# Optimization experiments

Measured on AMD Instinct MI355X. Metric: run time of the kernel, lower is better.

## Reference

```python
import jax, jax.numpy as jnp
import numpy as np

N = 10000      # nodes
E = 320000     # edges (avg degree 32)
D = 512        # input features
H = 2048       # dim_hidden hard-coded in module
C = 40         # num_classes


def setup_inputs() -> dict:
    key = jax.random.key(0)
    k = jax.random.split(key, 4)
    x = jax.random.normal(k[0], (N, D), dtype=jnp.float32)
    edge_index = jax.random.randint(k[1], (2, E), 0, N)
    W1 = jax.random.normal(k[2], (D, H), dtype=jnp.float32) * (1.0 / np.sqrt(D))
    b1 = jnp.zeros((H,), jnp.float32)
    W2 = jax.random.normal(k[3], (H, C), dtype=jnp.float32) * (1.0 / np.sqrt(H))
    b2 = jnp.zeros((C,), jnp.float32)
    return {"x": x, "edge_index": edge_index, "W1": W1, "b1": b1, "W2": W2, "b2": b2}


def _sym_norm(edge_index, n):
    # GCN symmetric normalization with self-loops: deg includes the self loop.
    src, dst = edge_index[0], edge_index[1]
    deg = jnp.zeros((n,), jnp.float32).at[dst].add(1.0) + 1.0
    dinv = jax.lax.rsqrt(deg)
    return src, dst, dinv


def _propagate(h, src, dst, dinv):
    # out[i] = sum_{j->i} dinv[j]*dinv[i]*h[j]  +  dinv[i]^2 * h[i] (self loop)
    coef = (dinv[src] * dinv[dst])[:, None]            # [E,1]
    agg = jax.ops.segment_sum(h[src] * coef, dst, num_segments=h.shape[0])
    return agg + h * (dinv * dinv)[:, None]


def _gcn_conv(x, W, b, src, dst, dinv):
    # A_hat (X W) == (A_hat X) W; aggregate in the smaller feature dim.
    if W.shape[0] <= W.shape[1]:
        return _propagate(x, src, dst, dinv) @ W + b
    return _propagate(x @ W, src, dst, dinv) + b


def reference(x, edge_index, W1, b1, W2, b2):
    src, dst, dinv = _sym_norm(edge_index, x.shape[0])
    h = jax.nn.relu(_gcn_conv(x, W1, b1, src, dst, dinv))
    return _gcn_conv(h, W2, b2, src, dst, dinv)
```

## Files before the change

kernel.cpp:

```cpp
#include <hip/hip_runtime.h>
#include <stdint.h>

#define N_NODES 10000
#define N_EDGES 320000
#define D_IN    512
#define D_HID   2048
#define N_CLS   40
#define MP1     10112
#define HSTR    136

typedef float f32x4  __attribute__((ext_vector_type(4)));
typedef short bf16x8 __attribute__((ext_vector_type(8)));
typedef unsigned short us8 __attribute__((ext_vector_type(8)));

__device__ inline unsigned short f2bf(float f){
  unsigned int u = __float_as_uint(f);
  u += 0x7fffu + ((u >> 16) & 1u);
  return (unsigned short)(u >> 16);
}

__device__ inline float bf2f(unsigned short h){
  return __uint_as_float(((unsigned int)h) << 16);
}

__device__ inline void gl_lds16(const void* g, void* l){
  __builtin_amdgcn_global_load_lds((const __attribute__((address_space(1))) void*)g,
                                   (__attribute__((address_space(3))) void*)l, 16, 0, 0);
}

__global__ void k_prep0(const float* __restrict__ x, unsigned short* __restrict__ Xb,
                        const int* __restrict__ ei, int* __restrict__ deg){
  if (blockIdx.x < 2500){
    int idx = blockIdx.x*256 + threadIdx.x;
    const f32x4* x4 = (const f32x4*)x;
    f32x4 a = x4[idx*2], b = x4[idx*2+1];
    us8 o;
    o[0]=f2bf(a.x); o[1]=f2bf(a.y); o[2]=f2bf(a.z); o[3]=f2bf(a.w);
    o[4]=f2bf(b.x); o[5]=f2bf(b.y); o[6]=f2bf(b.z); o[7]=f2bf(b.w);
    *(us8*)(Xb + (size_t)idx*8) = o;
  } else {
    int e = (blockIdx.x - 2500)*256 + threadIdx.x;
    if (e < N_EDGES) atomicAdd(&deg[ei[N_EDGES + e]], 1);
  }
}

__global__ void k_scan(const int* __restrict__ deg, int* __restrict__ offsets,
                       int* __restrict__ cursor, float* __restrict__ dinv){
  __shared__ int sums[1024];
  const int t = threadIdx.x;
  const int CH = 10;
  int base = t*CH;
  int local[CH]; int s = 0;
  for (int j = 0; j < CH; j++){
    int v = (base + j < N_NODES) ? deg[base + j] : 0;
    local[j] = s; s += v;
    if (base + j < N_NODES) dinv[base + j] = rsqrtf((float)v + 1.0f);
  }
  sums[t] = s;
  __syncthreads();
  for (int off = 1; off < 1024; off <<= 1){
    int v = (t >= off) ? sums[t - off] : 0;
    __syncthreads();
    sums[t] += v;
    __syncthreads();
  }
  int pre = (t > 0) ? sums[t-1] : 0;
  for (int j = 0; j < CH; j++){
    int idx = base + j;
    if (idx < N_NODES){ int o = pre + local[j]; offsets[idx] = o; cursor[idx] = o; }
  }
}

__global__ void k_fill(const int* __restrict__ ei, int* __restrict__ cursor, int* __restrict__ csr_src){
  int e = blockIdx.x*256 + threadIdx.x;
  if (e < N_EDGES){
    int s = ei[e], d = ei[N_EDGES + e];
    int pos = atomicAdd(&cursor[d], 1);
    csr_src[pos] = s;
  }
}

__global__ __launch_bounds__(256) void k_gjoint(const unsigned short* __restrict__ Xb,
                          const int* __restrict__ csr_src,
                          const int* __restrict__ offsets, const int* __restrict__ deg,
                          const float* __restrict__ dinv, unsigned short* __restrict__ Pb,
                          const float* __restrict__ W1, unsigned short* __restrict__ Wt1,
                          const float* __restrict__ W2, unsigned short* __restrict__ Wt2){
  __shared__ float tile[32][33];
  if (blockIdx.x < 2500){
    const int w    = threadIdx.x >> 6;
    const int lane = threadIdx.x & 63;
    const int i    = blockIdx.x*4 + w;
    const float di = dinv[i];
    float acc[8];
    us8 xi = *(const us8*)(Xb + (size_t)i*D_IN + lane*8);
    const float dii = di*di;
    #pragma unroll
    for (int r = 0; r < 8; r++) acc[r] = dii * bf2f(xi[r]);
    const int start = offsets[i], cnt = deg[i];
    for (int c0 = 0; c0 < cnt; c0 += 64){
      int m = cnt - c0; if (m > 64) m = 64;
      int s = 0; float cf = 0.0f;
      if (lane < m){ s = csr_src[start + c0 + lane]; cf = dinv[s]*di; }
      for (int j = 0; j < m; j++){
        int   sj = __shfl(s, j);
        float cj = __shfl(cf, j);
        us8 xr = *(const us8*)(Xb + (size_t)sj*D_IN + lane*8);
        #pragma unroll
        for (int r = 0; r < 8; r++) acc[r] += cj * bf2f(xr[r]);
      }
    }
    us8 o;
    #pragma unroll
    for (int r = 0; r < 8; r++) o[r] = f2bf(acc[r]);
    *(us8*)(Pb + (size_t)i*D_IN + lane*8) = o;
  } else if (blockIdx.x < 2500 + 1024){
    const int bb = blockIdx.x - 2500;
    const int n0 = (bb & 63)*32, k0 = (bb >> 6)*32;
    const int tx = threadIdx.x & 31, ty = threadIdx.x >> 5;
    for (int i = 0; i < 32; i += 8)
      tile[ty+i][tx] = W1[(size_t)(k0+ty+i)*D_HID + n0+tx];
    __syncthreads();
    for (int i = 0; i < 32; i += 8)
      Wt1[(size_t)(n0+ty+i)*D_IN + k0+tx] = f2bf(tile[tx][ty+i]);
  } else {
    int idx = (blockIdx.x - 3524)*256 + threadIdx.x;
    if (idx < 48*D_HID){
      int n = idx >> 11, k = idx & (D_HID-1);
      Wt2[idx] = (n < N_CLS) ? f2bf(W2[k*N_CLS + n]) : (unsigned short)0;
    }
  }
}

__global__ __launch_bounds__(256) void k_gemm1f(const unsigned short* __restrict__ Pb,
                                                const unsigned short* __restrict__ Wt1,
                                                const float* __restrict__ b1,
                                                const unsigned short* __restrict__ Wt2,
                                                float* __restrict__ G){
  __shared__ short smem[128*HSTR];
  short* As = smem;
  short* Bs = smem + 4096;
  short* Hs = smem;
  const int t    = threadIdx.x;
  const int lane = t & 63;
  const int wid  = t >> 6;
  const int wm   = (wid >> 1)*64, wn = (wid & 1)*64;
  const int m0   = blockIdx.x*128, n0 = blockIdx.y*128;
  const int arow = t >> 2;
  const int akof = ((t & 3) ^ ((t >> 3) & 3))*8;
  const int fr   = lane & 15;
  const int q    = lane >> 4;
  const int sq8  = (q ^ ((fr >> 1) & 3))*8;
  f32x4 acc[4][4] = {};
  for (int kb = 0; kb < D_IN; kb += 32){
    gl_lds16(Pb  + (size_t)(m0 +      arow)*D_IN + kb + akof, As + t*8);
    gl_lds16(Pb  + (size_t)(m0 + 64 + arow)*D_IN + kb + akof, As + 2048 + t*8);
    gl_lds16(Wt1 + (size_t)(n0 +      arow)*D_IN + kb + akof, Bs + t*8);
    gl_lds16(Wt1 + (size_t)(n0 + 64 + arow)*D_IN + kb + akof, Bs + 2048 + t*8);
    __syncthreads();
    bf16x8 a[4], b[4];
    #pragma unroll
    for (int i = 0; i < 4; i++) a[i] = *(const bf16x8*)(As + (wm + i*16 + fr)*32 + sq8);
    #pragma unroll
    for (int j = 0; j < 4; j++) b[j] = *(const bf16x8*)(Bs + (wn + j*16 + fr)*32 + sq8);
    #pragma unroll
    for (int i = 0; i < 4; i++)
      #pragma unroll
      for (int j = 0; j < 4; j++)
        acc[i][j] = __builtin_amdgcn_mfma_f32_16x16x32_bf16(a[i], b[j], acc[i][j], 0, 0, 0);
    __syncthreads();
  }
  #pragma unroll
  for (int j = 0; j < 4; j++){
    int col = wn + j*16 + fr;
    float bias = b1[n0 + col];
    #pragma unroll
    for (int i = 0; i < 4; i++){
      int rbase = wm + i*16 + q*4;
      f32x4 v = acc[i][j];
      #pragma unroll
      for (int r = 0; r < 4; r++){
        float h = fmaxf(v[r] + bias, 0.0f);
        Hs[(rbase + r)*HSTR + col] = (short)f2bf(h);
      }
    }
  }
  __syncthreads();
  f32x4 acc2[2][3] = {};
  for (int ks = 0; ks < 4; ks++){
    bf16x8 a2[2];
    #pragma unroll
    for (int i2 = 0; i2 < 2; i2++)
      a2[i2] = *(const bf16x8*)(Hs + (wid*32 + i2*16 + fr)*HSTR + ks*32 + q*8);
    #pragma unroll
    for (int j2 = 0; j2 < 3; j2++){
      bf16x8 b2 = *(const bf16x8*)(Wt2 + (size_t)(j2*16 + fr)*D_HID + n0 + ks*32 + q*8);
      #pragma unroll
      for (int i2 = 0; i2 < 2; i2++)
        acc2[i2][j2] = __builtin_amdgcn_mfma_f32_16x16x32_bf16(a2[i2], b2, acc2[i2][j2], 0, 0, 0);
    }
  }
  #pragma unroll
  for (int j2 = 0; j2 < 3; j2++){
    int col = j2*16 + fr;
    if (col < N_CLS){
      #pragma unroll
      for (int i2 = 0; i2 < 2; i2++){
        int rbase = m0 + wid*32 + i2*16 + q*4;
        f32x4 v = acc2[i2][j2];
        #pragma unroll
        for (int r = 0; r < 4; r++){
          int row = rbase + r;
          if (row < N_NODES)
            atomicAdd(&G[row*N_CLS + col], v[r]);
        }
      }
    }
  }
}

__global__ void k_gather2(const float* __restrict__ G, const int* __restrict__ csr_src,
                          const int* __restrict__ offsets, const int* __restrict__ deg,
                          const float* __restrict__ dinv, const float* __restrict__ b2,
                          float* __restrict__ out){
  __shared__ int   ssrc[64];
  __shared__ float scoef[64];
  const int i = blockIdx.x;
  const int t = threadIdx.x;
  const float di = dinv[i];
  const int start = offsets[i], cnt = deg[i];
  float acc = 0.0f;
  if (t < N_CLS) acc = di*di * G[i*N_CLS + t];
  for (int c0 = 0; c0 < cnt; c0 += 64){
    int m = cnt - c0; if (m > 64) m = 64;
    if (t < m){
      int s = csr_src[start + c0 + t];
      ssrc[t] = s; scoef[t] = dinv[s]*di;
    }
    __syncthreads();
    if (t < N_CLS)
      for (int j = 0; j < m; j++)
        acc += scoef[j] * G[ssrc[j]*N_CLS + t];
    __syncthreads();
  }
  if (t < N_CLS) out[i*N_CLS + t] = acc + b2[t];
}

extern "C" void kernel_launch(void* const* d_in, const int* in_sizes, int n_in,
                              void* d_out, int out_size, void* d_ws, size_t ws_size,
                              hipStream_t stream){
  const float* x  = (const float*)d_in[0];
  const int*   ei = (const int*)d_in[1];
  const float* W1 = (const float*)d_in[2];
  const float* b1 = (const float*)d_in[3];
  const float* W2 = (const float*)d_in[4];
  const float* b2 = (const float*)d_in[5];
  float* out = (float*)d_out;

  char* ws = (char*)d_ws;
  size_t off = 0;
  auto alloc = [&](size_t bytes) -> void* {
    void* p = ws + off; off += (bytes + 255) & ~(size_t)255; return p;
  };
  int*   deg     = (int*)alloc((size_t)N_NODES*4);
  float* dinv    = (float*)alloc((size_t)N_NODES*4);
  int*   offsets = (int*)alloc((size_t)N_NODES*4);
  int*   cursor  = (int*)alloc((size_t)N_NODES*4);
  int*   csr     = (int*)alloc((size_t)N_EDGES*4);
  unsigned short* Xb  = (unsigned short*)alloc((size_t)N_NODES*D_IN*2);
  unsigned short* Pb  = (unsigned short*)alloc((size_t)MP1*D_IN*2);
  unsigned short* Wt1 = (unsigned short*)alloc((size_t)D_HID*D_IN*2);
  unsigned short* Wt2 = (unsigned short*)alloc((size_t)48*D_HID*2);
  float* G = (float*)alloc((size_t)N_NODES*N_CLS*4);

  hipMemsetAsync(deg, 0, (size_t)N_NODES*4, stream);
  hipMemsetAsync(G,   0, (size_t)N_NODES*N_CLS*4, stream);

  k_prep0<<<2500 + 1250, 256, 0, stream>>>(x, Xb, ei, deg);
  k_scan<<<1, 1024, 0, stream>>>(deg, offsets, cursor, dinv);
  k_fill<<<(N_EDGES+255)/256, 256, 0, stream>>>(ei, cursor, csr);
  k_gjoint<<<2500 + 1024 + 384, 256, 0, stream>>>(Xb, csr, offsets, deg, dinv, Pb,
                                                  W1, Wt1, W2, Wt2);
  k_gemm1f<<<dim3(MP1/128, D_IN*4/128), 256, 0, stream>>>(Pb, Wt1, b1, Wt2, G);
  k_gather2<<<N_NODES, 64, 0, stream>>>(G, csr, offsets, deg, dinv, b2, out);
}
```

Measured before the change: 253.5 us.

## Double-buffer GEMM1 LDS tiles with direct-to-LDS prefetch and partial vmcnt waits

The GEMM1 main loop now ping-pongs between two LDS buffers, issuing the global-to-LDS loads for the next k-slice before computing the current one. It waits with a partial vmcnt so only the older loads must land, and replaces __syncthreads with raw s_barrier plus compiler memory fences. The aim is to hide global load latency behind the MFMA work. It relies on hand-encoded waitcnt immediates and on the 128*HSTR shared buffer being large enough for two 8192-short stages, which adds correctness risk.

```diff
diff --git a/kernel.cpp b/kernel.cpp
--- a/kernel.cpp
+++ b/kernel.cpp
@@ -138,8 +138,6 @@
                                                 const unsigned short* __restrict__ Wt2,
                                                 float* __restrict__ G){
   __shared__ short smem[128*HSTR];
-  short* As = smem;
-  short* Bs = smem + 4096;
   short* Hs = smem;
   const int t    = threadIdx.x;
   const int lane = t & 63;
@@ -151,13 +149,36 @@
   const int fr   = lane & 15;
   const int q    = lane >> 4;
   const int sq8  = (q ^ ((fr >> 1) & 3))*8;
+
+  const unsigned short* ApA = Pb  + (size_t)(m0 +      arow)*D_IN + akof;
+  const unsigned short* ApB = Pb  + (size_t)(m0 + 64 + arow)*D_IN + akof;
+  const unsigned short* BpA = Wt1 + (size_t)(n0 +      arow)*D_IN + akof;
+  const unsigned short* BpB = Wt1 + (size_t)(n0 + 64 + arow)*D_IN + akof;
+
   f32x4 acc[4][4] = {};
-  for (int kb = 0; kb < D_IN; kb += 32){
-    gl_lds16(Pb  + (size_t)(m0 +      arow)*D_IN + kb + akof, As + t*8);
-    gl_lds16(Pb  + (size_t)(m0 + 64 + arow)*D_IN + kb + akof, As + 2048 + t*8);
-    gl_lds16(Wt1 + (size_t)(n0 +      arow)*D_IN + kb + akof, Bs + t*8);
-    gl_lds16(Wt1 + (size_t)(n0 + 64 + arow)*D_IN + kb + akof, Bs + 2048 + t*8);
-    __syncthreads();
+  {
+    short* As = smem;       short* Bs = smem + 4096;
+    gl_lds16(ApA, As + t*8);  gl_lds16(ApB, As + 2048 + t*8);
+    gl_lds16(BpA, Bs + t*8);  gl_lds16(BpB, Bs + 2048 + t*8);
+  }
+  #pragma unroll
+  for (int ks = 0; ks < 16; ks++){
+    if (ks < 15){
+      short* As = smem + ((ks+1)&1)*8192;
+      short* Bs = As + 4096;
+      const int kb = (ks+1)*32;
+      gl_lds16(ApA + kb, As + t*8);  gl_lds16(ApB + kb, As + 2048 + t*8);
+      gl_lds16(BpA + kb, Bs + t*8);  gl_lds16(BpB + kb, Bs + 2048 + t*8);
+      asm volatile("" ::: "memory");
+      __builtin_amdgcn_s_waitcnt(0x0F74);
+    } else {
+      asm volatile("" ::: "memory");
+      __builtin_amdgcn_s_waitcnt(0x0F70);
+    }
+    __builtin_amdgcn_s_barrier();
+    asm volatile("" ::: "memory");
+    const short* As = smem + (ks&1)*8192;
+    const short* Bs = As + 4096;
     bf16x8 a[4], b[4];
     #pragma unroll
     for (int i = 0; i < 4; i++) a[i] = *(const bf16x8*)(As + (wm + i*16 + fr)*32 + sq8);
@@ -168,7 +189,9 @@
       #pragma unroll
       for (int j = 0; j < 4; j++)
         acc[i][j] = __builtin_amdgcn_mfma_f32_16x16x32_bf16(a[i], b[j], acc[i][j], 0, 0, 0);
-    __syncthreads();
+    asm volatile("" ::: "memory");
+    __builtin_amdgcn_s_barrier();
+    asm volatile("" ::: "memory");
   }
   #pragma unroll
   for (int j = 0; j < 4; j++){
```

Measured after the change: 242.0 us. 4.5% less time.

## Pre-swizzle GEMM operands into MFMA fragment layout and load directly to registers

Applied to the files above, without the earlier changes.

The aggregation and weight-transpose kernels now write A and B operands in a layout that matches the MFMA register fragments. The first GEMM then reads them straight from global memory into registers with a one-step register prefetch, dropping the LDS staging and both per-iteration barriers. The grid is transposed so that blocks sharing a weight column tile run adjacently, and launch bounds now request 3 blocks per CU. The cost is that each operand element is loaded separately by every wave that needs it, so reuse moves from LDS to L2/L1 and global traffic rises.

```diff
diff --git a/kernel.cpp b/kernel.cpp
--- a/kernel.cpp
+++ b/kernel.cpp
@@ -21,11 +21,6 @@
 
 __device__ inline float bf2f(unsigned short h){
   return __uint_as_float(((unsigned int)h) << 16);
-}
-
-__device__ inline void gl_lds16(const void* g, void* l){
-  __builtin_amdgcn_global_load_lds((const __attribute__((address_space(1))) void*)g,
-                                   (__attribute__((address_space(3))) void*)l, 16, 0, 0);
 }
 
 __global__ void k_prep0(const float* __restrict__ x, unsigned short* __restrict__ Xb,
@@ -83,8 +78,8 @@
 __global__ __launch_bounds__(256) void k_gjoint(const unsigned short* __restrict__ Xb,
                           const int* __restrict__ csr_src,
                           const int* __restrict__ offsets, const int* __restrict__ deg,
-                          const float* __restrict__ dinv, unsigned short* __restrict__ Pb,
-                          const float* __restrict__ W1, unsigned short* __restrict__ Wt1,
+                          const float* __restrict__ dinv, unsigned short* __restrict__ Afrag,
+                          const float* __restrict__ W1, unsigned short* __restrict__ Bfrag,
                           const float* __restrict__ W2, unsigned short* __restrict__ Wt2){
   __shared__ float tile[32][33];
   if (blockIdx.x < 2500){
@@ -113,7 +108,9 @@
     us8 o;
     #pragma unroll
     for (int r = 0; r < 8; r++) o[r] = f2bf(acc[r]);
-    *(us8*)(Pb + (size_t)i*D_IN + lane*8) = o;
+    const int mt = i >> 4, fr = i & 15;
+    const int ks = lane >> 2, q = lane & 3;
+    *(us8*)(Afrag + ((size_t)(mt*16 + ks)*64 + q*16 + fr)*8) = o;
   } else if (blockIdx.x < 2500 + 1024){
     const int bb = blockIdx.x - 2500;
     const int n0 = (bb & 63)*32, k0 = (bb >> 6)*32;
@@ -121,8 +118,14 @@
     for (int i = 0; i < 32; i += 8)
       tile[ty+i][tx] = W1[(size_t)(k0+ty+i)*D_HID + n0+tx];
     __syncthreads();
-    for (int i = 0; i < 32; i += 8)
-      Wt1[(size_t)(n0+ty+i)*D_IN + k0+tx] = f2bf(tile[tx][ty+i]);
+    const int ks = k0 >> 5;
+    for (int i = 0; i < 32; i += 8){
+      int n = n0 + ty + i;
+      int k = k0 + tx;
+      int p = n >> 7, jt = (n >> 4) & 7, fr = n & 15;
+      int q = (tx >> 3) & 3, e = tx & 7;
+      Bfrag[((((size_t)p*16 + ks)*8 + jt)*64 + q*16 + fr)*8 + e] = f2bf(tile[tx][ty+i]);
+    }
   } else {
     int idx = (blockIdx.x - 3524)*256 + threadIdx.x;
     if (idx < 48*D_HID){
@@ -132,44 +135,53 @@
   }
 }
 
-__global__ __launch_bounds__(256) void k_gemm1f(const unsigned short* __restrict__ Pb,
-                                                const unsigned short* __restrict__ Wt1,
-                                                const float* __restrict__ b1,
-                                                const unsigned short* __restrict__ Wt2,
-                                                float* __restrict__ G){
-  __shared__ short smem[128*HSTR];
-  short* As = smem;
-  short* Bs = smem + 4096;
-  short* Hs = smem;
+__global__ __launch_bounds__(256, 3) void k_gemm1f(const unsigned short* __restrict__ Afrag,
+                                                   const unsigned short* __restrict__ Bfrag,
+                                                   const float* __restrict__ b1,
+                                                   const unsigned short* __restrict__ Wt2,
+                                                   float* __restrict__ G){
+  __shared__ short Hs[128*HSTR];
   const int t    = threadIdx.x;
   const int lane = t & 63;
   const int wid  = t >> 6;
   const int wm   = (wid >> 1)*64, wn = (wid & 1)*64;
-  const int m0   = blockIdx.x*128, n0 = blockIdx.y*128;
-  const int arow = t >> 2;
-  const int akof = ((t & 3) ^ ((t >> 3) & 3))*8;
+  const int m0   = blockIdx.y*128, n0 = blockIdx.x*128;
   const int fr   = lane & 15;
   const int q    = lane >> 4;
-  const int sq8  = (q ^ ((fr >> 1) & 3))*8;
+
+  const int mtb = (m0 + wm) >> 4;
+  const int p   = blockIdx.x;
+  const int jtb = wn >> 4;
+  const unsigned short* Aw = Afrag + (size_t)lane*8;
+  const unsigned short* Bw = Bfrag + (size_t)lane*8;
+
   f32x4 acc[4][4] = {};
-  for (int kb = 0; kb < D_IN; kb += 32){
-    gl_lds16(Pb  + (size_t)(m0 +      arow)*D_IN + kb + akof, As + t*8);
-    gl_lds16(Pb  + (size_t)(m0 + 64 + arow)*D_IN + kb + akof, As + 2048 + t*8);
-    gl_lds16(Wt1 + (size_t)(n0 +      arow)*D_IN + kb + akof, Bs + t*8);
-    gl_lds16(Wt1 + (size_t)(n0 + 64 + arow)*D_IN + kb + akof, Bs + 2048 + t*8);
-    __syncthreads();
-    bf16x8 a[4], b[4];
-    #pragma unroll
-    for (int i = 0; i < 4; i++) a[i] = *(const bf16x8*)(As + (wm + i*16 + fr)*32 + sq8);
-    #pragma unroll
-    for (int j = 0; j < 4; j++) b[j] = *(const bf16x8*)(Bs + (wn + j*16 + fr)*32 + sq8);
+  bf16x8 ac[4], bc[4], an[4], bn[4];
+  #pragma unroll
+  for (int i = 0; i < 4; i++) ac[i] = *(const bf16x8*)(Aw + (size_t)(mtb + i)*8192);
+  #pragma unroll
+  for (int j = 0; j < 4; j++) bc[j] = *(const bf16x8*)(Bw + (size_t)((p*16 + 0)*8 + jtb + j)*512);
+
+  for (int ks = 0; ks < 16; ks++){
+    if (ks < 15){
+      #pragma unroll
+      for (int i = 0; i < 4; i++)
+        an[i] = *(const bf16x8*)(Aw + (size_t)((mtb + i)*16 + ks + 1)*512);
+      #pragma unroll
+      for (int j = 0; j < 4; j++)
+        bn[j] = *(const bf16x8*)(Bw + (size_t)((p*16 + ks + 1)*8 + jtb + j)*512);
+    }
     #pragma unroll
     for (int i = 0; i < 4; i++)
       #pragma unroll
       for (int j = 0; j < 4; j++)
-        acc[i][j] = __builtin_amdgcn_mfma_f32_16x16x32_bf16(a[i], b[j], acc[i][j], 0, 0, 0);
-    __syncthreads();
-  }
+        acc[i][j] = __builtin_amdgcn_mfma_f32_16x16x32_bf16(ac[i], bc[j], acc[i][j], 0, 0, 0);
+    #pragma unroll
+    for (int i = 0; i < 4; i++) ac[i] = an[i];
+    #pragma unroll
+    for (int j = 0; j < 4; j++) bc[j] = bn[j];
+  }
+
   #pragma unroll
   for (int j = 0; j < 4; j++){
     int col = wn + j*16 + fr;
@@ -267,10 +279,10 @@
   int*   offsets = (int*)alloc((size_t)N_NODES*4);
   int*   cursor  = (int*)alloc((size_t)N_NODES*4);
   int*   csr     = (int*)alloc((size_t)N_EDGES*4);
-  unsigned short* Xb  = (unsigned short*)alloc((size_t)N_NODES*D_IN*2);
-  unsigned short* Pb  = (unsigned short*)alloc((size_t)MP1*D_IN*2);
-  unsigned short* Wt1 = (unsigned short*)alloc((size_t)D_HID*D_IN*2);
-  unsigned short* Wt2 = (unsigned short*)alloc((size_t)48*D_HID*2);
+  unsigned short* Xb    = (unsigned short*)alloc((size_t)N_NODES*D_IN*2);
+  unsigned short* Afrag = (unsigned short*)alloc((size_t)(MP1/16)*16*64*8*2);
+  unsigned short* Bfrag = (unsigned short*)alloc((size_t)16*16*8*64*8*2);
+  unsigned short* Wt2   = (unsigned short*)alloc((size_t)48*D_HID*2);
   float* G = (float*)alloc((size_t)N_NODES*N_CLS*4);
 
   hipMemsetAsync(deg, 0, (size_t)N_NODES*4, stream);
@@ -279,8 +291,8 @@
   k_prep0<<<2500 + 1250, 256, 0, stream>>>(x, Xb, ei, deg);
   k_scan<<<1, 1024, 0, stream>>>(deg, offsets, cursor, dinv);
   k_fill<<<(N_EDGES+255)/256, 256, 0, stream>>>(ei, cursor, csr);
-  k_gjoint<<<2500 + 1024 + 384, 256, 0, stream>>>(Xb, csr, offsets, deg, dinv, Pb,
-                                                  W1, Wt1, W2, Wt2);
-  k_gemm1f<<<dim3(MP1/128, D_IN*4/128), 256, 0, stream>>>(Pb, Wt1, b1, Wt2, G);
+  k_gjoint<<<2500 + 1024 + 384, 256, 0, stream>>>(Xb, csr, offsets, deg, dinv, Afrag,
+                                                  W1, Bfrag, W2, Wt2);
+  k_gemm1f<<<dim3(D_HID/128, MP1/128), 256, 0, stream>>>(Afrag, Bfrag, b1, Wt2, G);
   k_gather2<<<N_NODES, 64, 0, stream>>>(G, csr, offsets, deg, dinv, b2, out);
 }
```

Result: faster. 247.2 us (-2.5%).
